# Performance work log

Hardware: AMD Instinct MI355X
Metric: run time of the kernel (lower is better)

## Reference

```python
import jax, jax.numpy as jnp
import numpy as np

B, S, D = 4, 2048, 1024
H = 4 * D          # expert hidden dim
E_SPEC = 4         # num specific experts
E_SHR = 2          # num shared experts
TOP_K = 2


def setup_inputs() -> dict:
    key = jax.random.key(0)
    ks = jax.random.split(key, 16)
    s = 0.02
    return {
        "x": jax.random.normal(ks[0], (B, S, D), jnp.float32),
        # specific experts (stacked over expert axis)
        "spec_w1": jax.random.normal(ks[1], (E_SPEC, D, H), jnp.float32) * s,
        "spec_b1": jnp.zeros((E_SPEC, H), jnp.float32),
        "spec_w2": jax.random.normal(ks[2], (E_SPEC, H, D), jnp.float32) * s,
        "spec_b2": jnp.zeros((E_SPEC, D), jnp.float32),
        "spec_rw": jax.random.normal(ks[3], (D, E_SPEC), jnp.float32) * s,
        "spec_rb": jnp.zeros((E_SPEC,), jnp.float32),
        # shared experts
        "shr_w1": jax.random.normal(ks[4], (E_SHR, D, H), jnp.float32) * s,
        "shr_b1": jnp.zeros((E_SHR, H), jnp.float32),
        "shr_w2": jax.random.normal(ks[5], (E_SHR, H, D), jnp.float32) * s,
        "shr_b2": jnp.zeros((E_SHR, D), jnp.float32),
        "shr_rw": jax.random.normal(ks[6], (D, E_SHR), jnp.float32) * s,
        "shr_rb": jnp.zeros((E_SHR,), jnp.float32),
    }


def _expert_mlp(xf, w1, b1, w2, b2):
    # xf: [T, D]; w1: [E, D, H]; w2: [E, H, D] -> [E, T, D]
    h = jax.nn.gelu(jnp.einsum("td,edh->eth", xf, w1) + b1[:, None, :],
                    approximate=False)
    return jnp.einsum("eth,ehd->etd", h, w2) + b2[:, None, :]


def reference(x, spec_w1, spec_b1, spec_w2, spec_b2, spec_rw, spec_rb,
              shr_w1, shr_b1, shr_w2, shr_b2, shr_rw, shr_rb):
    b, s, d = x.shape
    xf = x.reshape(-1, d)                      # [T, D]
    T = xf.shape[0]

    # --- specific (top-k) routing ---
    spec_probs = jax.nn.softmax(xf @ spec_rw + spec_rb, axis=-1)   # [T, E]
    topk_probs, topk_idx = jax.lax.top_k(spec_probs, TOP_K)        # [T, K]

    # aux load-balancing loss
    counts = jnp.zeros((E_SPEC,), jnp.float32).at[topk_idx.reshape(-1)].add(1.0)
    fraction = counts / (T * TOP_K)
    aux_loss = E_SPEC * jnp.sum(fraction * spec_probs.mean(axis=0))

    # gate[t, e] = sum_k topk_probs[t,k] * 1[topk_idx[t,k]==e]
    gate = jnp.sum(jax.nn.one_hot(topk_idx, E_SPEC, dtype=xf.dtype)
                   * topk_probs[..., None], axis=1)                # [T, E]

    spec_out_e = _expert_mlp(xf, spec_w1, spec_b1, spec_w2, spec_b2)  # [E, T, D]
    specific_out = jnp.einsum("te,etd->td", gate, spec_out_e)

    # --- shared (dense) experts ---
    shr_probs = jax.nn.softmax(xf @ shr_rw + shr_rb, axis=-1)      # [T, E_shr]
    shr_out_e = _expert_mlp(xf, shr_w1, shr_b1, shr_w2, shr_b2)    # [E_shr, T, D]
    shared_out = jnp.einsum("te,etd->td", shr_probs, shr_out_e)

    final = (specific_out + shared_out).reshape(b, s, d)
    return final, aux_loss
```

## Files before the change

### kernel.cpp

```cpp
#include <hip/hip_runtime.h>
#include <hip/hip_bf16.h>

#define T_TOK 8192
#define DDIM 1024
#define HDIM 4096

typedef __bf16 bf16;
typedef bf16 bf16x8 __attribute__((ext_vector_type(8)));
typedef float f32x4 __attribute__((ext_vector_type(4)));

#define ASM_VMCNT(n) asm volatile("s_waitcnt vmcnt(" #n ")" ::: "memory")
#define MFMA16(a, b, c) __builtin_amdgcn_mfma_f32_16x16x32_bf16((a), (b), (c), 0, 0, 0)

__device__ __forceinline__ void gl_lds16(const void* g, void* l) {
  __builtin_amdgcn_global_load_lds(
      (const __attribute__((address_space(1))) unsigned int*)g,
      (__attribute__((address_space(3))) unsigned int*)l, 16, 0, 0);
}

__global__ __launch_bounds__(256) void convert_x(const float* __restrict__ x,
                                                 bf16* __restrict__ xb) {
  const size_t i = ((size_t)blockIdx.x * 256 + threadIdx.x) * 8;
  const float4 v0 = *(const float4*)(x + i);
  const float4 v1 = *(const float4*)(x + i + 4);
  bf16x8 o;
  o[0] = (bf16)v0.x; o[1] = (bf16)v0.y; o[2] = (bf16)v0.z; o[3] = (bf16)v0.w;
  o[4] = (bf16)v1.x; o[5] = (bf16)v1.y; o[6] = (bf16)v1.z; o[7] = (bf16)v1.w;
  *(bf16x8*)(xb + i) = o;
}

__global__ __launch_bounds__(256) void transpose_convert(
    const float* __restrict__ src, bf16* __restrict__ dst, int R, int C) {
  __shared__ float tile[32][33];
  const size_t mat = (size_t)blockIdx.z * R * C;
  const int c0 = blockIdx.x * 32, r0 = blockIdx.y * 32;
  const int tx = threadIdx.x & 31, ty = threadIdx.x >> 5;
#pragma unroll
  for (int i = 0; i < 4; ++i)
    tile[ty + 8 * i][tx] =
        src[mat + (size_t)(r0 + ty + 8 * i) * C + c0 + tx];
  __syncthreads();
#pragma unroll
  for (int i = 0; i < 4; ++i)
    dst[mat + (size_t)(c0 + ty + 8 * i) * R + r0 + tx] =
        (bf16)tile[tx][ty + 8 * i];
}

__global__ __launch_bounds__(256) void router_probs(
    const float* __restrict__ x, const float* __restrict__ srw,
    const float* __restrict__ srb, const float* __restrict__ hrw,
    const float* __restrict__ hrb, float* __restrict__ gate,
    float4* __restrict__ probs4, int* __restrict__ top2) {
  const int lane = threadIdx.x & 63;
  const int w = threadIdx.x >> 6;
  const int t = blockIdx.x * 4 + w;

  const float* xr = x + (size_t)t * DDIM;
  float p0 = 0, p1 = 0, p2 = 0, p3 = 0, p4 = 0, p5 = 0;
#pragma unroll
  for (int c = 0; c < 4; ++c) {
    const int d = c * 256 + lane * 4;
    const float4 xv = *(const float4*)(xr + d);
    const float xa[4] = {xv.x, xv.y, xv.z, xv.w};
#pragma unroll
    for (int j = 0; j < 4; ++j) {
      const float xd = xa[j];
      const float4 r4 = *(const float4*)(srw + (size_t)(d + j) * 4);
      p0 += xd * r4.x; p1 += xd * r4.y; p2 += xd * r4.z; p3 += xd * r4.w;
      const float2 r2 = *(const float2*)(hrw + (size_t)(d + j) * 2);
      p4 += xd * r2.x; p5 += xd * r2.y;
    }
  }
#pragma unroll
  for (int off = 32; off >= 1; off >>= 1) {
    p0 += __shfl_xor(p0, off);
    p1 += __shfl_xor(p1, off);
    p2 += __shfl_xor(p2, off);
    p3 += __shfl_xor(p3, off);
    p4 += __shfl_xor(p4, off);
    p5 += __shfl_xor(p5, off);
  }
  if (lane == 0) {
    const float l0 = p0 + srb[0], l1 = p1 + srb[1];
    const float l2 = p2 + srb[2], l3 = p3 + srb[3];
    const float m = fmaxf(fmaxf(l0, l1), fmaxf(l2, l3));
    const float e0 = expf(l0 - m), e1 = expf(l1 - m);
    const float e2 = expf(l2 - m), e3 = expf(l3 - m);
    const float s = e0 + e1 + e2 + e3;
    float pr[4] = {e0 / s, e1 / s, e2 / s, e3 / s};
    int i1 = 0; float v1 = pr[0];
#pragma unroll
    for (int e = 1; e < 4; ++e) if (pr[e] > v1) { v1 = pr[e]; i1 = e; }
    int i2 = -1; float v2 = -1.0f;
#pragma unroll
    for (int e = 0; e < 4; ++e)
      if (e != i1 && pr[e] > v2) { v2 = pr[e]; i2 = e; }
    float g[4] = {0, 0, 0, 0};
    g[i1] = v1; g[i2] = v2;
    float* gr = gate + (size_t)t * 8;
    gr[0] = g[0]; gr[1] = g[1]; gr[2] = g[2]; gr[3] = g[3];
    const float h0 = p4 + hrb[0], h1 = p5 + hrb[1];
    const float mh = fmaxf(h0, h1);
    const float q0 = expf(h0 - mh), q1 = expf(h1 - mh);
    const float qs = q0 + q1;
    gr[4] = q0 / qs; gr[5] = q1 / qs; gr[6] = 0; gr[7] = 0;
    probs4[t] = make_float4(pr[0], pr[1], pr[2], pr[3]);
    top2[t] = i1 | (i2 << 8);
  }
}

__global__ __launch_bounds__(1024) void scan_build(
    const int* __restrict__ top2, const float4* __restrict__ probs4,
    int* __restrict__ cnt, int* __restrict__ lists, float* __restrict__ auxg) {
  __shared__ unsigned long long sc[1024];
  __shared__ float4 rp[512];
  const int tid = threadIdx.x;

  int ee[8];
  unsigned long long c = 0;
  float4 ps = make_float4(0.f, 0.f, 0.f, 0.f);
#pragma unroll
  for (int j = 0; j < 8; ++j) {
    const int t = tid * 8 + j;
    const int p = top2[t];
    ee[j] = p;
    const int a = p & 15, b = (p >> 8) & 15;
    c += (1ULL << (16 * a)) + (1ULL << (16 * b));
    const float4 pv = probs4[t];
    ps.x += pv.x; ps.y += pv.y; ps.z += pv.z; ps.w += pv.w;
  }
  sc[tid] = c;
  __syncthreads();
  for (int off = 1; off < 1024; off <<= 1) {
    const unsigned long long mine = sc[tid];
    const unsigned long long prev = (tid >= off) ? sc[tid - off] : 0ULL;
    __syncthreads();
    sc[tid] = mine + prev;
    __syncthreads();
  }
  const unsigned long long incl = sc[tid];
  const unsigned long long tot = sc[1023];
  const unsigned long long excl = incl - c;
  int q0 = (int)(excl & 0xffff), q1 = (int)((excl >> 16) & 0xffff);
  int q2 = (int)((excl >> 32) & 0xffff), q3 = (int)((excl >> 48) & 0xffff);
#pragma unroll
  for (int j = 0; j < 8; ++j) {
    const int t = tid * 8 + j;
    const int a = ee[j] & 15, b = (ee[j] >> 8) & 15;
    const int pa = (a == 0) ? q0 : (a == 1) ? q1 : (a == 2) ? q2 : q3;
    lists[a * 8192 + pa] = t;
    q0 += (a == 0); q1 += (a == 1); q2 += (a == 2); q3 += (a == 3);
    const int pb = (b == 0) ? q0 : (b == 1) ? q1 : (b == 2) ? q2 : q3;
    lists[b * 8192 + pb] = t;
    q0 += (b == 0); q1 += (b == 1); q2 += (b == 2); q3 += (b == 3);
  }
  if (tid == 1023) {
    const int c0 = (int)(tot & 0xffff), c1 = (int)((tot >> 16) & 0xffff);
    const int c2 = (int)((tot >> 32) & 0xffff), c3 = (int)((tot >> 48) & 0xffff);
    cnt[0] = c0; cnt[1] = c1; cnt[2] = c2; cnt[3] = c3;
    auxg[0] = (float)c0; auxg[1] = (float)c1;
    auxg[2] = (float)c2; auxg[3] = (float)c3;
  }
  if (tid >= 512) rp[tid - 512] = ps;
  __syncthreads();
  if (tid < 512) {
    const float4 o = rp[tid];
    ps.x += o.x; ps.y += o.y; ps.z += o.z; ps.w += o.w;
  }
  for (int w = 256; w >= 1; w >>= 1) {
    __syncthreads();
    if (tid >= w && tid < 2 * w) rp[tid - w] = ps;
    __syncthreads();
    if (tid < w) {
      const float4 o = rp[tid];
      ps.x += o.x; ps.y += o.y; ps.z += o.z; ps.w += o.w;
    }
  }
  if (tid == 0) {
    auxg[4] = ps.x; auxg[5] = ps.y; auxg[6] = ps.z; auxg[7] = ps.w;
  }
}

__global__ void aux_finalize(const float* __restrict__ auxg,
                             float* __restrict__ outp) {
  float a = 0.0f;
#pragma unroll
  for (int e = 0; e < 4; ++e)
    a += (auxg[e] / (float)(T_TOK * 2)) * (auxg[4 + e] / (float)T_TOK);
  outp[0] = 4.0f * a;
}

template <int MODE>
__global__ __launch_bounds__(256, 3) void gemmv(
    const bf16* __restrict__ A, const bf16* __restrict__ B, int N, int K,
    const float* __restrict__ bias, bf16* __restrict__ Hout, int NBn,
    int CH_M, int CH_N, const int* __restrict__ cnt,
    const int* __restrict__ lists, int eid) {
  __shared__ __align__(1024) bf16 As[128 * 32];
  __shared__ __align__(1024) bf16 Bs[128 * 32];

  const int tid = threadIdx.x;
  const int lane = tid & 63, wid = tid >> 6;
  const int wm = wid >> 1, wn = wid & 1;
  const int lr = lane & 15, lg = lane >> 4;

  int bm, bn;
  if constexpr (MODE == 4) {
    const int nbm = ((cnt[eid] + 127) & ~127) >> 7;
    const int CHm = (nbm + 3) >> 2;
    const int need = 8 * CHm * CH_N;
    if (blockIdx.x >= need) return;
    const int xc = blockIdx.x & 7;
    const int idx = blockIdx.x >> 3;
    bm = (xc >> 1) * CHm + idx / CH_N;
    bn = (xc & 1) * CH_N + idx % CH_N;
    if (bm >= nbm) return;
  } else {
    const int xcd = blockIdx.x & 7;
    const int idx = blockIdx.x >> 3;
    const int ncn = NBn / CH_N;
    bm = (xcd / ncn) * CH_M + idx / CH_N;
    bn = (xcd % ncn) * CH_N + idx % CH_N;
  }

  const int rl = tid >> 2;
  const int c = ((tid & 3) * 16) ^ (((rl >> 1) & 3) << 4);
  int ar0 = bm * 128 + rl, ar1 = ar0 + 64;
  if constexpr (MODE == 4) {
    const int* lp = lists + eid * 8192;
    int t = lp[ar0]; ar0 = t < 0 ? 0 : t;
    t = lp[ar1]; ar1 = t < 0 ? 0 : t;
  }
  const bf16* sA0 = A + (size_t)ar0 * K + (c >> 1);
  const bf16* sA1 = A + (size_t)ar1 * K + (c >> 1);
  const bf16* sB0 = B + (size_t)(bn * 128 + rl) * K + (c >> 1);
  const bf16* sB1 = B + (size_t)(bn * 128 + 64 + rl) * K + (c >> 1);
  char* const dA0 = (char*)As + wid * 1024;
  char* const dA1 = (char*)As + 4096 + wid * 1024;
  char* const dB0 = (char*)Bs + wid * 1024;
  char* const dB1 = (char*)Bs + 4096 + wid * 1024;

  const int rkey = ((lr >> 1) & 3) << 4;
  const char* Ard = (const char*)As + (wm * 64 + lr) * 64 + ((lg * 16) ^ rkey);
  const char* Brd = (const char*)Bs + (wn * 64 + lr) * 64 + ((lg * 16) ^ rkey);

  f32x4 acc[4][4] = {};
  const int NT = K >> 5;
  for (int kt = 0; kt < NT; ++kt) {
    const int ko = kt << 5;
    gl_lds16(sA0 + ko, dA0);
    gl_lds16(sA1 + ko, dA1);
    gl_lds16(sB0 + ko, dB0);
    gl_lds16(sB1 + ko, dB1);
    __syncthreads();
    bf16x8 af[4], bfr[4];
#pragma unroll
    for (int mf = 0; mf < 4; ++mf) af[mf] = *(const bf16x8*)(Ard + mf * 1024);
#pragma unroll
    for (int nf = 0; nf < 4; ++nf) bfr[nf] = *(const bf16x8*)(Brd + nf * 1024);
    __builtin_amdgcn_s_setprio(1);
#pragma unroll
    for (int mf = 0; mf < 4; ++mf)
#pragma unroll
      for (int nf = 0; nf < 4; ++nf)
        acc[mf][nf] = MFMA16(af[mf], bfr[nf], acc[mf][nf]);
    __builtin_amdgcn_s_setprio(0);
    __syncthreads();
  }

  const int colb = bn * 128 + wn * 64;
  const int rowb = bm * 128 + wm * 64 + lg * 4;
  float bv[4];
#pragma unroll
  for (int nf = 0; nf < 4; ++nf) bv[nf] = bias[colb + nf * 16 + lr];
#pragma unroll
  for (int mf = 0; mf < 4; ++mf)
#pragma unroll
    for (int nf = 0; nf < 4; ++nf) {
      const int col = colb + nf * 16 + lr;
#pragma unroll
      for (int r = 0; r < 4; ++r) {
        const int row = rowb + mf * 16 + r;
        const float v = acc[mf][nf][r] + bv[nf];
        const float gl = 0.5f * v * (1.0f + erff(v * 0.7071067811865475f));
        Hout[(size_t)row * N + col] = (bf16)gl;
      }
    }
}

template <int BN_, int MODE>
__global__ __launch_bounds__(512, 2) void gemm4p(
    const bf16* __restrict__ A, const bf16* __restrict__ B, int M, int N,
    int K, const float* __restrict__ bias, bf16* __restrict__ Hout,
    float* __restrict__ Fout, const float* __restrict__ gate, int gidx,
    int NBn, int CH_M, int CH_N, const int* __restrict__ cnt,
    const int* __restrict__ lists, int eid) {
  constexpr int NREP = BN_ / 64;
  constexpr int NHF = NREP / 2;
  constexpr int WNT = BN_ / 4;
  constexpr int ABYTES = 256 * 64 * 2;
  constexpr int BBYTES = BN_ * 64 * 2;
  constexpr bool DYN = (MODE == 3);

  __shared__ __align__(1024) bf16 Alds[2 * 256 * 64];
  __shared__ __align__(1024) bf16 Blds[2 * BN_ * 64];

  const int tid = threadIdx.x;
  const int lane = tid & 63, wid = tid >> 6;
  const int wm = wid >> 2, wn = wid & 3;
  const int lr = lane & 15, lg = lane >> 4;

  int bm, bn;
  if constexpr (DYN) {
    const int nbm = ((cnt[eid] + 255) & ~255) >> 8;
    const int CHm = (nbm + 3) >> 2;
    constexpr int CHn = (BN_ == 256) ? 8 : 4;
    const int need = 8 * CHm * CHn;
    if (blockIdx.x >= need) return;
    const int xc = blockIdx.x & 7;
    const int idx = blockIdx.x >> 3;
    bm = (xc >> 1) * CHm + idx / CHn;
    bn = (xc & 1) * CHn + idx % CHn;
    if (bm >= nbm) return;
  } else {
    const int xcd = blockIdx.x & 7;
    const int idx = blockIdx.x >> 3;
    const int ncn = NBn / CH_N;
    bm = (xcd / ncn) * CH_M + idx / CH_N;
    bn = (xcd % ncn) * CH_N + idx % CH_N;
  }

  const int NT = K >> 6;

  const int L = tid * 16;
  const int rl = L >> 7;
  const int colb = (L & 127) ^ ((rl & 7) << 4);

  const int ar0 = bm * 256 + rl;
  const bf16* sAc0 = A + (size_t)ar0 * K + (colb >> 1);
  const bf16* sAc1 = A + (size_t)(ar0 + 64) * K + (colb >> 1);
  const bf16* sAc2 = A + (size_t)(ar0 + 128) * K + (colb >> 1);
  const bf16* sAc3 = A + (size_t)(ar0 + 192) * K + (colb >> 1);
  const bf16* sB = B + (size_t)(bn * BN_ + rl) * K + (colb >> 1);

  char* const ldsA = (char*)Alds;
  char* const ldsB = (char*)Blds;
  const int wb = wid * 1024;
  char* const stA[2] = {ldsA + wb, ldsA + ABYTES + wb};
  char* const stB[2] = {ldsB + wb, ldsB + BBYTES + wb};

  const int ax0 = (lg * 16) ^ ((lr & 7) << 4);
  const int ax1 = ax0 ^ 64;
  const int aro = (wm * 128 + lr) * 128;
  const int bro = (wn * WNT + lr) * 128;
  const char* const Ak0[2] = {ldsA + aro + ax0, ldsA + ABYTES + aro + ax0};
  const char* const Ak1[2] = {ldsA + aro + ax1, ldsA + ABYTES + aro + ax1};
  const char* const Bk0[2] = {ldsB + bro + ax0, ldsB + BBYTES + bro + ax0};
  const char* const Bk1[2] = {ldsB + bro + ax1, ldsB + BBYTES + bro + ax1};

  f32x4 acc[8][NREP] = {};

  gl_lds16(sAc0, stA[0]);
  gl_lds16(sAc1, stA[0] + 8192);
  gl_lds16(sAc2, stA[0] + 16384);
  gl_lds16(sAc3, stA[0] + 24576);
  gl_lds16(sB, stB[0]);
  gl_lds16(sB + (size_t)64 * K, stB[0] + 8192);
  if constexpr (BN_ == 256) {
    gl_lds16(sB + (size_t)128 * K, stB[0] + 16384);
    gl_lds16(sB + (size_t)192 * K, stB[0] + 24576);
  }
  gl_lds16(sB + 64, stB[1]);
  gl_lds16(sB + (size_t)64 * K + 64, stB[1] + 8192);
  if constexpr (BN_ == 256) {
    gl_lds16(sB + (size_t)128 * K + 64, stB[1] + 16384);
    gl_lds16(sB + (size_t)192 * K + 64, stB[1] + 24576);
  }
  gl_lds16(sAc0 + 64, stA[1]);
  gl_lds16(sAc1 + 64, stA[1] + 8192);
  if constexpr (BN_ == 256) ASM_VMCNT(6); else ASM_VMCNT(4);
  __builtin_amdgcn_s_barrier();

  for (int kt0 = 0; kt0 < NT; kt0 += 2) {
#pragma unroll
    for (int par = 0; par < 2; ++par) {
      const int kt = kt0 + par;
      const int cur = par, oth = par ^ 1;
      const bool st1 = (kt + 1) < NT, st2 = (kt + 2) < NT;
      const size_t ko1 = (size_t)(kt + 1) << 6, ko2 = (size_t)(kt + 2) << 6;
      const char* Ac0 = Ak0[cur]; const char* Ac1 = Ak1[cur];
      const char* Bc0 = Bk0[cur]; const char* Bc1 = Bk1[cur];

      bf16x8 af[4][2], bfr[NREP][2];

#pragma unroll
      for (int mf = 0; mf < 4; ++mf) {
        af[mf][0] = *(const bf16x8*)(Ac0 + mf * 2048);
        af[mf][1] = *(const bf16x8*)(Ac1 + mf * 2048);
      }
#pragma unroll
      for (int nf = 0; nf < NHF; ++nf) {
        bfr[nf][0] = *(const bf16x8*)(Bc0 + nf * 2048);
        bfr[nf][1] = *(const bf16x8*)(Bc1 + nf * 2048);
      }
      if (st1) {
        gl_lds16(sAc2 + ko1, stA[oth] + 16384);
        gl_lds16(sAc3 + ko1, stA[oth] + 24576);
      }
      __builtin_amdgcn_s_barrier();
      asm volatile("s_waitcnt lgkmcnt(0)" ::: "memory");
      __builtin_amdgcn_sched_barrier(0);
      __builtin_amdgcn_s_setprio(1);
#pragma unroll
      for (int mf = 0; mf < 4; ++mf)
#pragma unroll
        for (int nf = 0; nf < NHF; ++nf) {
          acc[mf][nf] = MFMA16(af[mf][0], bfr[nf][0], acc[mf][nf]);
          acc[mf][nf] = MFMA16(af[mf][1], bfr[nf][1], acc[mf][nf]);
        }
      __builtin_amdgcn_s_setprio(0);
      __builtin_amdgcn_s_barrier();

#pragma unroll
      for (int nf = NHF; nf < NREP; ++nf) {
        bfr[nf][0] = *(const bf16x8*)(Bc0 + nf * 2048);
        bfr[nf][1] = *(const bf16x8*)(Bc1 + nf * 2048);
      }
      __builtin_amdgcn_s_barrier();
      asm volatile("s_waitcnt lgkmcnt(0)" ::: "memory");
      __builtin_amdgcn_sched_barrier(0);
      __builtin_amdgcn_s_setprio(1);
#pragma unroll
      for (int mf = 0; mf < 4; ++mf)
#pragma unroll
        for (int nf = NHF; nf < NREP; ++nf) {
          acc[mf][nf] = MFMA16(af[mf][0], bfr[nf][0], acc[mf][nf]);
          acc[mf][nf] = MFMA16(af[mf][1], bfr[nf][1], acc[mf][nf]);
        }
      __builtin_amdgcn_s_setprio(0);
      __builtin_amdgcn_s_barrier();

#pragma unroll
      for (int mf = 0; mf < 4; ++mf) {
        af[mf][0] = *(const bf16x8*)(Ac0 + 8192 + mf * 2048);
        af[mf][1] = *(const bf16x8*)(Ac1 + 8192 + mf * 2048);
      }
      if (st2) {
        gl_lds16(sB + ko2, stB[cur]);
        gl_lds16(sB + (size_t)64 * K + ko2, stB[cur] + 8192);
      }
      __builtin_amdgcn_s_barrier();
      asm volatile("s_waitcnt lgkmcnt(0)" ::: "memory");
      __builtin_amdgcn_sched_barrier(0);
      __builtin_amdgcn_s_setprio(1);
#pragma unroll
      for (int mf = 0; mf < 4; ++mf)
#pragma unroll
        for (int nf = 0; nf < NHF; ++nf) {
          acc[4 + mf][nf] = MFMA16(af[mf][0], bfr[nf][0], acc[4 + mf][nf]);
          acc[4 + mf][nf] = MFMA16(af[mf][1], bfr[nf][1], acc[4 + mf][nf]);
        }
      __builtin_amdgcn_s_setprio(0);
      __builtin_amdgcn_s_barrier();

      if (st2) {
        if constexpr (BN_ == 256) {
          gl_lds16(sB + (size_t)128 * K + ko2, stB[cur] + 16384);
          gl_lds16(sB + (size_t)192 * K + ko2, stB[cur] + 24576);
        }
        gl_lds16(sAc0 + ko2, stA[cur]);
        gl_lds16(sAc1 + ko2, stA[cur] + 8192);
      }
      __builtin_amdgcn_s_setprio(1);
#pragma unroll
      for (int mf = 0; mf < 4; ++mf)
#pragma unroll
        for (int nf = NHF; nf < NREP; ++nf) {
          acc[4 + mf][nf] = MFMA16(af[mf][0], bfr[nf][0], acc[4 + mf][nf]);
          acc[4 + mf][nf] = MFMA16(af[mf][1], bfr[nf][1], acc[4 + mf][nf]);
        }
      __builtin_amdgcn_s_setprio(0);
      if (st2) {
        if constexpr (BN_ == 256) ASM_VMCNT(6); else ASM_VMCNT(4);
        __builtin_amdgcn_s_barrier();
      } else if (st1) {
        ASM_VMCNT(0);
        __builtin_amdgcn_s_barrier();
      }
    }
  }

  const int colb2 = bn * BN_ + wn * WNT;
  const int rowb = bm * 256 + wm * 128 + lg * 4;
  float bv[NREP];
#pragma unroll
  for (int nf = 0; nf < NREP; ++nf) bv[nf] = bias[colb2 + nf * 16 + lr];
#pragma unroll
  for (int mf = 0; mf < 8; ++mf) {
    if constexpr (MODE == 1 || MODE == 2) {
      float gv[4];
#pragma unroll
      for (int r = 0; r < 4; ++r)
        gv[r] = gate[(size_t)(rowb + mf * 16 + r) * 8 + gidx];
#pragma unroll
      for (int nf = 0; nf < NREP; ++nf) {
        const int col = colb2 + nf * 16 + lr;
#pragma unroll
        for (int r = 0; r < 4; ++r) {
          const float v = acc[mf][nf][r] + bv[nf];
          const size_t oi = (size_t)(rowb + mf * 16 + r) * N + col;
          if constexpr (MODE == 1)
            Fout[oi] += gv[r] * v;
          else
            Fout[oi] = gv[r] * v;
        }
      }
    } else {
      const int* lp = lists + eid * 8192;
      int tok[4]; float gv[4];
#pragma unroll
      for (int r = 0; r < 4; ++r) {
        tok[r] = lp[rowb + mf * 16 + r];
        gv[r] = tok[r] >= 0 ? gate[(size_t)tok[r] * 8 + gidx] : 0.0f;
      }
#pragma unroll
      for (int nf = 0; nf < NREP; ++nf) {
        const int col = colb2 + nf * 16 + lr;
#pragma unroll
        for (int r = 0; r < 4; ++r) {
          if (tok[r] >= 0) {
            const float v = acc[mf][nf][r] + bv[nf];
            Fout[(size_t)tok[r] * N + col] += gv[r] * v;
          }
        }
      }
    }
  }
}

extern "C" void kernel_launch(void* const* d_in, const int* in_sizes, int n_in,
                              void* d_out, int out_size, void* d_ws,
                              size_t ws_size, hipStream_t stream) {
  const float* x = (const float*)d_in[0];
  const float* spec_w1 = (const float*)d_in[1];
  const float* spec_b1 = (const float*)d_in[2];
  const float* spec_w2 = (const float*)d_in[3];
  const float* spec_b2 = (const float*)d_in[4];
  const float* spec_rw = (const float*)d_in[5];
  const float* spec_rb = (const float*)d_in[6];
  const float* shr_w1 = (const float*)d_in[7];
  const float* shr_b1 = (const float*)d_in[8];
  const float* shr_w2 = (const float*)d_in[9];
  const float* shr_b2 = (const float*)d_in[10];
  const float* shr_rw = (const float*)d_in[11];
  const float* shr_rb = (const float*)d_in[12];
  float* out = (float*)d_out;

  char* ws = (char*)d_ws;
  const size_t OFF_W1 = 16777216;
  const size_t OFF_W2 = OFF_W1 + 50331648;
  const size_t OFF_H = OFF_W2 + 50331648;
  const size_t OFF_GATE = OFF_H + 67108864;
  const size_t OFF_AUX = OFF_GATE + 262144;
  const size_t OFF_CNT = OFF_AUX + 64;
  const size_t OFF_LIST = OFF_CNT + 64;
  const size_t OFF_T2 = OFF_LIST + 131072;
  const size_t OFF_P4 = OFF_T2 + 32768;
  bf16* xb = (bf16*)ws;
  bf16* w1t = (bf16*)(ws + OFF_W1);
  bf16* w2t = (bf16*)(ws + OFF_W2);
  bf16* hbuf = (bf16*)(ws + OFF_H);
  float* gate = (float*)(ws + OFF_GATE);
  float* auxg = (float*)(ws + OFF_AUX);
  int* cnt = (int*)(ws + OFF_CNT);
  int* lists = (int*)(ws + OFF_LIST);
  int* top2 = (int*)(ws + OFF_T2);
  float4* probs4 = (float4*)(ws + OFF_P4);

  hipMemsetAsync(lists, 0xFF, 4 * 8192 * 4, stream);

  convert_x<<<(T_TOK * DDIM) / 2048, 256, 0, stream>>>(x, xb);
  transpose_convert<<<dim3(HDIM / 32, DDIM / 32, 4), 256, 0, stream>>>(
      spec_w1, w1t, DDIM, HDIM);
  transpose_convert<<<dim3(HDIM / 32, DDIM / 32, 2), 256, 0, stream>>>(
      shr_w1, w1t + (size_t)4 * DDIM * HDIM, DDIM, HDIM);
  transpose_convert<<<dim3(DDIM / 32, HDIM / 32, 4), 256, 0, stream>>>(
      spec_w2, w2t, HDIM, DDIM);
  transpose_convert<<<dim3(DDIM / 32, HDIM / 32, 2), 256, 0, stream>>>(
      shr_w2, w2t + (size_t)4 * DDIM * HDIM, HDIM, DDIM);

  router_probs<<<T_TOK / 4, 256, 0, stream>>>(x, spec_rw, spec_rb, shr_rw,
                                              shr_rb, gate, probs4, top2);
  scan_build<<<1, 1024, 0, stream>>>(top2, probs4, cnt, lists, auxg);

  for (int es = 0; es < 2; ++es) {
    const bf16* w1e = w1t + (size_t)(4 + es) * DDIM * HDIM;
    const bf16* w2e = w2t + (size_t)(4 + es) * DDIM * HDIM;
    const float* b1e = shr_b1 + (size_t)es * HDIM;
    const float* b2e = shr_b2 + (size_t)es * DDIM;
    gemmv<0><<<2048, 256, 0, stream>>>(xb, w1e, HDIM, DDIM, b1e, hbuf,
                                       32, 16, 16, nullptr, nullptr, 0);
    if (es == 0)
      gemm4p<128, 2><<<256, 512, 0, stream>>>(
          hbuf, w2e, T_TOK, DDIM, HDIM, b2e, nullptr, out, gate, 4,
          8, 8, 4, nullptr, nullptr, 0);
    else
      gemm4p<128, 1><<<256, 512, 0, stream>>>(
          hbuf, w2e, T_TOK, DDIM, HDIM, b2e, nullptr, out, gate, 5,
          8, 8, 4, nullptr, nullptr, 0);
  }

  for (int e = 0; e < 4; ++e) {
    const bf16* w1e = w1t + (size_t)e * DDIM * HDIM;
    const bf16* w2e = w2t + (size_t)e * DDIM * HDIM;
    const float* b1e = spec_b1 + (size_t)e * HDIM;
    const float* b2e = spec_b2 + (size_t)e * DDIM;
    gemmv<4><<<2048, 256, 0, stream>>>(xb, w1e, HDIM, DDIM, b1e, hbuf,
                                       32, 0, 16, cnt, lists, e);
    gemm4p<128, 3><<<256, 512, 0, stream>>>(
        hbuf, w2e, T_TOK, DDIM, HDIM, b2e, nullptr, out, gate, e,
        8, 0, 0, cnt, lists, e);
  }
  aux_finalize<<<1, 1, 0, stream>>>(auxg, out + (size_t)T_TOK * DDIM);
}
```

Measured before the change: 1.059 ms.

## Triple-buffer gemmv LDS loads and use polynomial erf approximation in GELU

Turns the single-buffered K loop of the gemmv kernel into a three-stage ring of LDS buffers. Global-to-LDS loads are issued three tiles ahead and gated by vmcnt waits and barriers, so memory latency overlaps the MFMA work. The GELU epilogue also replaces erff with an Abramowitz-Stegun polynomial plus __expf to make the epilogue cheaper. The costs are triple the LDS footprint, which may limit occupancy at 3 blocks per CU, and a small accuracy loss in erf (about 1e-7 absolute), which is negligible after rounding to bf16.

```diff
diff --git a/kernel.cpp b/kernel.cpp
--- a/kernel.cpp
+++ b/kernel.cpp
@@ -16,6 +16,21 @@
   __builtin_amdgcn_global_load_lds(
       (const __attribute__((address_space(1))) unsigned int*)g,
       (__attribute__((address_space(3))) unsigned int*)l, 16, 0, 0);
+}
+
+__device__ __forceinline__ float gelu_f(float v) {
+  const float x = v * 0.7071067811865475f;
+  const float ax = fabsf(x);
+  const float t = 1.0f / fmaf(0.3275911f, ax, 1.0f);
+  float p = fmaf(1.061405429f, t, -1.453152027f);
+  p = fmaf(p, t, 1.421413741f);
+  p = fmaf(p, t, -0.284496736f);
+  p = fmaf(p, t, 0.254829592f);
+  p = p * t;
+  const float e = __expf(-ax * ax);
+  const float er = fmaf(-p, e, 1.0f);
+  const float erfx = (x >= 0.0f) ? er : -er;
+  return 0.5f * v * (1.0f + erfx);
 }
 
 __global__ __launch_bounds__(256) void convert_x(const float* __restrict__ x,
@@ -196,8 +211,8 @@
     const float* __restrict__ bias, bf16* __restrict__ Hout, int NBn,
     int CH_M, int CH_N, const int* __restrict__ cnt,
     const int* __restrict__ lists, int eid) {
-  __shared__ __align__(1024) bf16 As[128 * 32];
-  __shared__ __align__(1024) bf16 Bs[128 * 32];
+  __shared__ __align__(1024) bf16 As[3 * 128 * 32];
+  __shared__ __align__(1024) bf16 Bs[3 * 128 * 32];
 
   const int tid = threadIdx.x;
   const int lane = tid & 63, wid = tid >> 6;
@@ -246,26 +261,48 @@
 
   f32x4 acc[4][4] = {};
   const int NT = K >> 5;
-  for (int kt = 0; kt < NT; ++kt) {
-    const int ko = kt << 5;
-    gl_lds16(sA0 + ko, dA0);
-    gl_lds16(sA1 + ko, dA1);
-    gl_lds16(sB0 + ko, dB0);
-    gl_lds16(sB1 + ko, dB1);
-    __syncthreads();
-    bf16x8 af[4], bfr[4];
-#pragma unroll
-    for (int mf = 0; mf < 4; ++mf) af[mf] = *(const bf16x8*)(Ard + mf * 1024);
-#pragma unroll
-    for (int nf = 0; nf < 4; ++nf) bfr[nf] = *(const bf16x8*)(Brd + nf * 1024);
-    __builtin_amdgcn_s_setprio(1);
-#pragma unroll
-    for (int mf = 0; mf < 4; ++mf)
-#pragma unroll
-      for (int nf = 0; nf < 4; ++nf)
-        acc[mf][nf] = MFMA16(af[mf], bfr[nf], acc[mf][nf]);
-    __builtin_amdgcn_s_setprio(0);
-    __syncthreads();
+
+#define GV_STAGE(KO, SLOT)                    \
+  gl_lds16(sA0 + (KO), dA0 + (SLOT)*8192);    \
+  gl_lds16(sA1 + (KO), dA1 + (SLOT)*8192);    \
+  gl_lds16(sB0 + (KO), dB0 + (SLOT)*8192);    \
+  gl_lds16(sB1 + (KO), dB1 + (SLOT)*8192);
+  GV_STAGE(0, 0)
+  GV_STAGE(32, 1)
+  GV_STAGE(64, 2)
+  ASM_VMCNT(8);
+  __builtin_amdgcn_s_barrier();
+
+#define GV_ITER(KT, SLOT)                                                  \
+  {                                                                        \
+    bf16x8 af[4], bfr[4];                                                  \
+    _Pragma("unroll") for (int mf = 0; mf < 4; ++mf)                       \
+        af[mf] = *(const bf16x8*)(Ard + (SLOT)*8192 + mf * 1024);          \
+    _Pragma("unroll") for (int nf = 0; nf < 4; ++nf)                       \
+        bfr[nf] = *(const bf16x8*)(Brd + (SLOT)*8192 + nf * 1024);         \
+    asm volatile("s_waitcnt lgkmcnt(0)" ::: "memory");                     \
+    __builtin_amdgcn_s_setprio(1);                                         \
+    _Pragma("unroll") for (int mf = 0; mf < 4; ++mf)                       \
+        _Pragma("unroll") for (int nf = 0; nf < 4; ++nf)                   \
+            acc[mf][nf] = MFMA16(af[mf], bfr[nf], acc[mf][nf]);            \
+    __builtin_amdgcn_s_setprio(0);                                         \
+    __builtin_amdgcn_s_barrier();                                          \
+    if ((KT) + 3 < NT) {                                                   \
+      const int ko_ = ((KT) + 3) << 5;                                     \
+      GV_STAGE(ko_, SLOT)                                                  \
+      ASM_VMCNT(8);                                                        \
+    } else if ((KT) + 2 < NT) {                                            \
+      ASM_VMCNT(4);                                                        \
+    } else if ((KT) + 1 < NT) {                                            \
+      ASM_VMCNT(0);                                                        \
+    }                                                                      \
+    __builtin_amdgcn_s_barrier();                                          \
+  }
+
+  for (int kt0 = 0; kt0 < NT; kt0 += 3) {
+    GV_ITER(kt0, 0)
+    if (kt0 + 1 < NT) GV_ITER(kt0 + 1, 1)
+    if (kt0 + 2 < NT) GV_ITER(kt0 + 2, 2)
   }
 
   const int colb = bn * 128 + wn * 64;
@@ -281,9 +318,7 @@
 #pragma unroll
       for (int r = 0; r < 4; ++r) {
         const int row = rowb + mf * 16 + r;
-        const float v = acc[mf][nf][r] + bv[nf];
-        const float gl = 0.5f * v * (1.0f + erff(v * 0.7071067811865475f));
-        Hout[(size_t)row * N + col] = (bf16)gl;
+        Hout[(size_t)row * N + col] = (bf16)gelu_f(acc[mf][nf][r] + bv[nf]);
       }
     }
 }
```

Result: no change. 1.045 ms (-1.4%).
